# Kernel optimization log

Hardware: AMD Instinct MI355X
Metric: run time of the kernel (lower is better)

Reference implementation:

```python
import jax, jax.numpy as jnp
import numpy as np

DEPTH_BINS = 64
TEMPERATURE = 1.0


def _conv2d(x, w, b, pad):
    y = jax.lax.conv_general_dilated(x, w, (1, 1), [(pad, pad), (pad, pad)],
                                     dimension_numbers=('NCHW', 'OIHW', 'NCHW'))
    return y + b[None, :, None, None]


def _conv3d(x, w, b, pad):
    y = jax.lax.conv_general_dilated(x, w, (1, 1, 1), [(pad, pad)] * 3,
                                     dimension_numbers=('NCDHW', 'OIDHW', 'NCDHW'))
    return y + b[None, :, None, None, None]


def setup_inputs() -> dict:
    key = jax.random.key(0)
    ks = jax.random.split(key, 16)
    B, N, C, H, W = 2, 5, 256, 96, 96
    s = 0.05  # weight scale
    return {
        'focal_features': jax.random.normal(ks[0], (B, N, C, H, W), jnp.float32),
        'focus_distances': jax.random.uniform(ks[1], (B, N), jnp.float32, 0.5, 5.0),
        'camera_encoding': jax.random.normal(ks[2], (B, 16), jnp.float32),
        'W1': jax.random.normal(ks[3], (256, 512, 3, 3), jnp.float32) * s,
        'b1': jnp.zeros((256,), jnp.float32),
        'W2': jax.random.normal(ks[4], (128, 256, 3, 3), jnp.float32) * s,
        'b2': jnp.zeros((128,), jnp.float32),
        'W3': jax.random.normal(ks[5], (1, 128, 1, 1), jnp.float32) * s,
        'b3': jnp.zeros((1,), jnp.float32),
        'R1': jax.random.normal(ks[6], (32, 64, 3, 3, 3), jnp.float32) * s,
        'rb1': jnp.zeros((32,), jnp.float32),
        'R2': jax.random.normal(ks[7], (16, 32, 3, 3, 3), jnp.float32) * s,
        'rb2': jnp.zeros((16,), jnp.float32),
        'R3': jax.random.normal(ks[8], (64, 16, 1, 1, 1), jnp.float32) * s,
        'rb3': jnp.zeros((64,), jnp.float32),
    }


def reference(focal_features, focus_distances, camera_encoding,
              W1, b1, W2, b2, W3, b3, R1, rb1, R2, rb2, R3, rb3):
    B, N, C, H, W = focal_features.shape
    # _apply_blur is identity and depth only affects the (unused) blur sigma,
    # so the per-depth matching cost is identical across all depth bins.
    feat_ref = focal_features[:, 0]  # [B,C,H,W]
    pair = jnp.concatenate(
        [focal_features, jnp.broadcast_to(feat_ref[:, None], focal_features.shape)],
        axis=2)  # [B,N,2C,H,W]
    x = pair.reshape(B * N, 2 * C, H, W)
    x = jax.nn.relu(_conv2d(x, W1, b1, 1))
    x = jax.nn.relu(_conv2d(x, W2, b2, 1))
    cost = _conv2d(x, W3, b3, 0)  # [B*N,1,H,W]
    cost_agg = cost.reshape(B, N, H, W).mean(axis=1)  # [B,H,W]
    # identical for every depth bin -> broadcast
    cv = jnp.broadcast_to(cost_agg[:, None], (B, DEPTH_BINS, H, W))
    # refine_net: Conv3d over channels=depth_bins, spatial dims (H, W, 1)
    v = cv[..., None]  # [B, depth_bins, H, W, 1]
    v = jax.nn.relu(_conv3d(v, R1, rb1, 1))
    v = jax.nn.relu(_conv3d(v, R2, rb2, 1))
    v = _conv3d(v, R3, rb3, 0)  # [B, depth_bins, H, W, 1]
    cv_ref = v[..., 0]  # [B, depth_bins, H, W]
    depth_probs = jax.nn.softmax(-cv_ref / TEMPERATURE, axis=1)
    cost_volume = jnp.transpose(cv_ref, (0, 2, 3, 1))   # [B,H,W,depth_bins]
    depth_probs = jnp.transpose(depth_probs, (0, 2, 3, 1))
    return cost_volume, depth_probs
```

## Files before the change

### kernel.cpp

```cpp
#include <hip/hip_runtime.h>
#include <stdint.h>

typedef unsigned short u16;
typedef _Float16 f16;
typedef _Float16 f16x8 __attribute__((ext_vector_type(8)));
typedef float    f32x4 __attribute__((ext_vector_type(4)));

#define HW   96
#define NPIX (HW*HW)
#define BBATCH 2
#define NVIEW  5
#define NIMG 10

#define ASTR 80
#define LDS_B_OFF 7840
#define LDS_BYTES (7840 + 30720)

__device__ __forceinline__ u16 f16u(float f) {
    union { u16 u; f16 h; } v; v.h = (f16)f; return v.u;
}

__global__ __launch_bounds__(256)
void k_prep_w(const float* __restrict__ W1, const float* __restrict__ W2,
              const float* __restrict__ R1, const float* __restrict__ R2, const float* __restrict__ R3,
              u16* __restrict__ w1a, u16* __restrict__ w1b, u16* __restrict__ w2t,
              float* __restrict__ s1t, float* __restrict__ s2t, float* __restrict__ r3t)
{
    int id = blockIdx.x * 256 + threadIdx.x;
    if (id < 589824) {
        int t = id >> 16; int r = id & 65535; int o = r >> 8; int c = r & 255;
        int kh = t / 3, kw = t % 3;
        *(f16*)&w1a[id] = (f16)W1[((size_t)(o * 512 + c) * 3 + kh) * 3 + kw];
        *(f16*)&w1b[id] = (f16)W1[((size_t)(o * 512 + 256 + c) * 3 + kh) * 3 + kw];
        return;
    }
    id -= 589824;
    if (id < 294912) {
        int t = id >> 15; int r = id & 32767; int o = r >> 8; int c = r & 255;
        *(f16*)&w2t[id] = (f16)W2[((size_t)(o * 256 + c) * 3 + t / 3) * 3 + (t % 3)];
        return;
    }
    id -= 294912;
    if (id < 288) {
        int t = id >> 5; int o = id & 31;
        float s = 0.f;
        for (int i = 0; i < 64; ++i)
            s += R1[((size_t)((o * 64 + i) * 3 + t / 3) * 3 + t % 3) * 3 + 1];
        s1t[id] = s;
        return;
    }
    id -= 288;
    if (id < 4608) {
        int o = id & 15; int r = id >> 4; int i = r & 31; int t = r >> 5;
        s2t[id] = R2[((size_t)((o * 32 + i) * 3 + t / 3) * 3 + t % 3) * 3 + 1];
        return;
    }
    id -= 4608;
    if (id < 1024) {
        int o = id & 63; int i = id >> 6;
        r3t[id] = R3[(size_t)o * 16 + i];
    }
}

__global__ __launch_bounds__(256)
void k_tr(const float* __restrict__ src, u16* __restrict__ dst, int img0, int imgMul)
{
    const int cblk = blockIdx.x, row = blockIdx.y, z = blockIdx.z;
    const int gimg = img0 + z * imgMul;
    const int tid = threadIdx.x;
    __shared__ u16 tile[96 * 40];
    const int c = tid >> 3, j = tid & 7;
    const float* s = src + ((size_t)(gimg * 256 + cblk * 32 + c)) * NPIX + (size_t)row * HW + j * 12;
    #pragma unroll
    for (int k = 0; k < 3; ++k) {
        const float4 v = ((const float4*)s)[k];
        const int px = j * 12 + k * 4;
        tile[(px + 0) * 40 + c] = f16u(v.x);
        tile[(px + 1) * 40 + c] = f16u(v.y);
        tile[(px + 2) * 40 + c] = f16u(v.z);
        tile[(px + 3) * 40 + c] = f16u(v.w);
    }
    __syncthreads();
    if (tid < 192) {
        const int px = tid >> 1, part = tid & 1;
        const uint4 v0 = ((const uint4*)(tile + px * 40 + part * 16))[0];
        const uint4 v1 = ((const uint4*)(tile + px * 40 + part * 16))[1];
        uint4* d = (uint4*)(dst + ((((size_t)z * HW + row) * 8 + cblk) * HW + px) * 32 + part * 16);
        d[0] = v0; d[1] = v1;
    }
}

template<int MODE>
__global__ __launch_bounds__(256, 4)
void k_conv(const u16* __restrict__ in, const u16* __restrict__ wt,
            const u16* __restrict__ refp, const float* __restrict__ bias,
            const float* __restrict__ W3, void* __restrict__ outp, int ib)
{
    constexpr int Cout = (MODE == 2) ? 128 : 256;
    const int h  = blockIdx.x;
    const int y  = blockIdx.y;
    const int ob = blockIdx.z * 128;
    const int tid = threadIdx.x;
    const int wv = tid >> 6, l = tid & 63;
    const int wm = wv >> 1, wn = wv & 1;
    const int lane16 = l & 15, quad = l >> 4;

    __shared__ __align__(16) char lds[LDS_BYTES];

    f32x4 acc[3][4];
    #pragma unroll
    for (int mf = 0; mf < 3; ++mf)
        #pragma unroll
        for (int nf = 0; nf < 4; ++nf) acc[mf][nf] = (f32x4){0.f, 0.f, 0.f, 0.f};

    if (tid < 32) {
        const int base = (tid >> 4) ? 97 * ASTR : 0;
        ((unsigned int*)(lds + base))[tid & 15] = 0u;
    }

    for (int dh = -1; dh <= 1; ++dh) {
        const int hh = h + dh;
        if ((unsigned)hh >= (unsigned)HW) continue;
        for (int c0 = 0; c0 < 256; c0 += 32) {
            __syncthreads();
            if (tid < 192) {
                const int px = tid >> 1, half = tid & 1;
                const uint4* g = (const uint4*)(in +
                    ((((size_t)y * HW + hh) * 8 + (c0 >> 5)) * HW + px) * 32 + half * 16);
                const uint4 v0 = g[0], v1 = g[1];
                uint4* d = (uint4*)(lds + (px + 1) * ASTR + half * 32);
                d[0] = v0; d[1] = v1;
            }
            #pragma unroll
            for (int i = 0; i < 3; ++i) {
                const int idx = i * 256 + tid;
                const int dwt = idx >> 8, o = (idx >> 1) & 127, half = idx & 1;
                const int tap = (dh + 1) * 3 + dwt;
                const uint4* g = (const uint4*)(wt +
                    ((size_t)tap * Cout + ob + o) * 256 + c0 + half * 16);
                const uint4 v0 = g[0], v1 = g[1];
                uint4* d = (uint4*)(lds + LDS_B_OFF + (dwt * 128 + o) * ASTR + half * 32);
                d[0] = v0; d[1] = v1;
            }
            __syncthreads();
            #pragma unroll
            for (int dw = 0; dw < 3; ++dw) {
                f16x8 af[3];
                #pragma unroll
                for (int mf = 0; mf < 3; ++mf)
                    af[mf] = *(const f16x8*)(lds + (wm * 48 + mf * 16 + lane16 + dw) * ASTR + quad * 16);
                #pragma unroll
                for (int nf = 0; nf < 4; ++nf) {
                    const f16x8 bf = *(const f16x8*)(lds + LDS_B_OFF +
                        (dw * 128 + wn * 64 + nf * 16 + lane16) * ASTR + quad * 16);
                    #pragma unroll
                    for (int mf = 0; mf < 3; ++mf)
                        acc[mf][nf] = __builtin_amdgcn_mfma_f32_16x16x32_f16(af[mf], bf, acc[mf][nf], 0, 0, 0);
                }
            }
        }
    }

    if (MODE <= 1) {
        const int rimg = (MODE == 1) ? (ib + y) / NVIEW : 0;
        float bias4[4] = {0.f, 0.f, 0.f, 0.f};
        if (MODE == 1) {
            #pragma unroll
            for (int nf = 0; nf < 4; ++nf) bias4[nf] = bias[ob + wn * 64 + nf * 16 + lane16];
        }
        char* epi = lds + wv * 3072;
        u16* outg = (u16*)outp;
        #pragma unroll
        for (int p = 0; p < 2; ++p) {
            __syncthreads();
            #pragma unroll
            for (int nn = 0; nn < 2; ++nn) {
                const int nf = p * 2 + nn;
                #pragma unroll
                for (int mf = 0; mf < 3; ++mf)
                    #pragma unroll
                    for (int r = 0; r < 4; ++r) {
                        const int pxl = mf * 16 + quad * 4 + r;
                        *(u16*)(epi + pxl * 64 + (nn * 16 + lane16) * 2) =
                            f16u(acc[mf][nf][r] + bias4[nf]);
                    }
            }
            __syncthreads();
            const int cblk = (ob + wn * 64 + p * 32) >> 5;
            const size_t obase = (((size_t)y * HW + h) * 8 + cblk) * (size_t)(HW * 32);
            const size_t rbase = (((size_t)rimg * HW + h) * 8 + cblk) * (size_t)(HW * 32);
            #pragma unroll
            for (int i = 0; i < 3; ++i) {
                const int u = i * 64 + l;
                const int pxl = u >> 2, part = u & 3;
                f16x8 v = *(const f16x8*)(epi + pxl * 64 + part * 16);
                const int px = wm * 48 + pxl;
                if (MODE == 1) {
                    const f16x8 rv = *(const f16x8*)(refp + rbase + (size_t)px * 32 + part * 8);
                    #pragma unroll
                    for (int jj = 0; jj < 8; ++jj)
                        v[jj] = (f16)fmaxf((float)v[jj] + (float)rv[jj], 0.f);
                }
                *(f16x8*)(outg + obase + (size_t)px * 32 + part * 8) = v;
            }
        }
    } else {
        const int gimg = ib + y;
        float w3v[4], b2v[4];
        #pragma unroll
        for (int nf = 0; nf < 4; ++nf) {
            const int o = wn * 64 + nf * 16 + lane16;
            w3v[nf] = W3[o]; b2v[nf] = bias[o];
        }
        float s[3][4];
        #pragma unroll
        for (int mf = 0; mf < 3; ++mf)
            #pragma unroll
            for (int r = 0; r < 4; ++r) {
                float t = 0.f;
                #pragma unroll
                for (int nf = 0; nf < 4; ++nf)
                    t += w3v[nf] * fmaxf(acc[mf][nf][r] + b2v[nf], 0.f);
                s[mf][r] = t;
            }
        #pragma unroll
        for (int xb = 1; xb < 16; xb <<= 1)
            #pragma unroll
            for (int mf = 0; mf < 3; ++mf)
                #pragma unroll
                for (int r = 0; r < 4; ++r)
                    s[mf][r] += __shfl_xor(s[mf][r], xb);
        __syncthreads();
        float* cs = (float*)lds;
        if (wn == 0 && lane16 == 0) {
            #pragma unroll
            for (int mf = 0; mf < 3; ++mf)
                #pragma unroll
                for (int r = 0; r < 4; ++r)
                    cs[wm * 48 + mf * 16 + quad * 4 + r] = s[mf][r];
        }
        __syncthreads();
        if (wn == 1 && lane16 == 0) {
            float* pvp = (float*)outp + (size_t)gimg * NPIX + (size_t)h * HW;
            #pragma unroll
            for (int mf = 0; mf < 3; ++mf)
                #pragma unroll
                for (int r = 0; r < 4; ++r) {
                    const int px = wm * 48 + mf * 16 + quad * 4 + r;
                    pvp[px] = cs[px] + s[mf][r];
                }
        }
    }
}

__global__ __launch_bounds__(256)
void k_cost_sum(const float* __restrict__ pv, const float* __restrict__ b3, float* __restrict__ ca)
{
    const int id = blockIdx.x * 256 + threadIdx.x;
    if (id >= BBATCH * NPIX) return;
    const int b = id / NPIX, hw = id % NPIX;
    float s = 0.f;
    #pragma unroll
    for (int n = 0; n < NVIEW; ++n) s += pv[(size_t)(b * NVIEW + n) * NPIX + hw];
    ca[id] = b3[0] + 0.2f * s;
}

__global__ __launch_bounds__(256)
void k_d1(const float* __restrict__ cost_agg, const float* __restrict__ s1t,
          const float* __restrict__ rb1, float* __restrict__ t1)
{
    const int id = blockIdx.x * 256 + threadIdx.x;
    const int o = id & 31; const int r = id >> 5;
    const int hw = r % NPIX; const int bimg = r / NPIX;
    const int y = hw / HW, x = hw % HW;
    const float* ca = cost_agg + (size_t)bimg * NPIX;
    float s = rb1[o];
    #pragma unroll
    for (int t = 0; t < 9; ++t) {
        const int yy = y + t / 3 - 1, xx = x + t % 3 - 1;
        if ((unsigned)yy < HW && (unsigned)xx < HW)
            s += s1t[t * 32 + o] * ca[yy * HW + xx];
    }
    t1[id] = fmaxf(s, 0.f);
}

__global__ __launch_bounds__(256)
void k_d2(const float* __restrict__ t1, const float* __restrict__ s2t,
          const float* __restrict__ rb2, float* __restrict__ t2)
{
    const int id = blockIdx.x * 256 + threadIdx.x;
    const int o = id & 15; const int r = id >> 4;
    const int hw = r % NPIX; const int bimg = r / NPIX;
    const int y = hw / HW, x = hw % HW;
    float s = rb2[o];
    for (int t = 0; t < 9; ++t) {
        const int yy = y + t / 3 - 1, xx = x + t % 3 - 1;
        if ((unsigned)yy < HW && (unsigned)xx < HW) {
            const float* tp = t1 + ((size_t)bimg * NPIX + yy * HW + xx) * 32;
            #pragma unroll
            for (int i = 0; i < 32; ++i)
                s += s2t[(t * 32 + i) * 16 + o] * tp[i];
        }
    }
    t2[id] = fmaxf(s, 0.f);
}

__global__ __launch_bounds__(256)
void k_d3(const float* __restrict__ t2, const float* __restrict__ r3t,
          const float* __restrict__ rb3, float* __restrict__ out)
{
    const int wv = threadIdx.x >> 6, o = threadIdx.x & 63;
    const int pix = blockIdx.x * 4 + wv;
    const float* tp = t2 + (size_t)pix * 16;
    float cv = rb3[o];
    #pragma unroll
    for (int i = 0; i < 16; ++i) cv += r3t[i * 64 + o] * tp[i];
    const float z = -cv;
    float m = z;
    #pragma unroll
    for (int off = 32; off; off >>= 1) m = fmaxf(m, __shfl_xor(m, off));
    const float e = __expf(z - m);
    float s = e;
    #pragma unroll
    for (int off = 32; off; off >>= 1) s += __shfl_xor(s, off);
    const float p = e / s;
    const size_t idx = (size_t)pix * 64 + o;
    out[idx] = cv;
    out[idx + (size_t)BBATCH * NPIX * 64] = p;
}

extern "C" void kernel_launch(void* const* d_in, const int* in_sizes, int n_in,
                              void* d_out, int out_size, void* d_ws, size_t ws_size,
                              hipStream_t stream)
{
    (void)in_sizes; (void)n_in; (void)out_size;
    const float* focal = (const float*)d_in[0];
    const float* W1  = (const float*)d_in[3];
    const float* b1  = (const float*)d_in[4];
    const float* W2  = (const float*)d_in[5];
    const float* b2  = (const float*)d_in[6];
    const float* W3  = (const float*)d_in[7];
    const float* b3  = (const float*)d_in[8];
    const float* R1  = (const float*)d_in[9];
    const float* rb1 = (const float*)d_in[10];
    const float* R2  = (const float*)d_in[11];
    const float* rb2 = (const float*)d_in[12];
    const float* R3  = (const float*)d_in[13];
    const float* rb3 = (const float*)d_in[14];

    char* ws = (char*)d_ws;
    size_t off = 0;
    auto alloc = [&](size_t sz) { char* p = ws + off; off = (off + sz + 255) & ~(size_t)255; return p; };
    const size_t IMG = (size_t)HW * 8 * HW * 32 * 2;
    u16*   w1a  = (u16*)  alloc(1179648);
    u16*   w1b  = (u16*)  alloc(1179648);
    u16*   w2t  = (u16*)  alloc(589824);
    float* s1t  = (float*)alloc(1152);
    float* s2t  = (float*)alloc(18432);
    float* r3t  = (float*)alloc(4096);
    float* ca   = (float*)alloc(73728);
    float* t1   = (float*)alloc(2359296);
    float* t2   = (float*)alloc(1179648);
    float* pv   = (float*)alloc(NIMG * NPIX * 4);
    u16*   refp   = (u16*)alloc(BBATCH * IMG);
    u16*   feats2 = (u16*)alloc(BBATCH * IMG);
    const size_t base = off;
    int C = 1;
    if (base + 20 * IMG + 512 <= ws_size)      C = 10;
    else if (base + 10 * IMG + 512 <= ws_size) C = 5;
    else if (base + 4 * IMG + 512 <= ws_size)  C = 2;
    u16* feats = (u16*)alloc((size_t)C * IMG);
    u16* x1    = (u16*)alloc((size_t)C * IMG);

    k_prep_w<<<(890656 + 255) / 256, 256, 0, stream>>>(W1, W2, R1, R2, R3, w1a, w1b, w2t, s1t, s2t, r3t);

    k_tr<<<dim3(8, HW, BBATCH), 256, 0, stream>>>(focal, feats2, 0, NVIEW);
    k_conv<0><<<dim3(HW, BBATCH, 2), 256, 0, stream>>>(feats2, w1b, nullptr, nullptr, nullptr, refp, 0);

    for (int ib = 0; ib < NIMG; ib += C) {
        k_tr<<<dim3(8, HW, C), 256, 0, stream>>>(focal, feats, ib, 1);
        k_conv<1><<<dim3(HW, C, 2), 256, 0, stream>>>(feats, w1a, refp, b1, nullptr, x1, ib);
        k_conv<2><<<dim3(HW, C, 1), 256, 0, stream>>>(x1, w2t, nullptr, b2, W3, pv, ib);
    }

    k_cost_sum<<<(BBATCH * NPIX + 255) / 256, 256, 0, stream>>>(pv, b3, ca);
    k_d1<<<(BBATCH * NPIX * 32) / 256, 256, 0, stream>>>(ca, s1t, rb1, t1);
    k_d2<<<(BBATCH * NPIX * 16) / 256, 256, 0, stream>>>(t1, s2t, rb2, t2);
    k_d3<<<(BBATCH * NPIX) / 4, 256, 0, stream>>>(t2, r3t, rb3, (float*)d_out);
}
```

Measured before the change: 471.2 us.

## Double-buffer activation tiles and read conv weights directly from global memory

The implicit-GEMM conv mainloop now keeps two LDS activation buffers. The next channel chunk is prefetched into registers while the MFMAs run, which removes one barrier per iteration. Weight fragments are no longer staged through LDS; each wave loads them directly from global memory (relying on L1/L2 reuse), which shrinks LDS from about 38KB to about 15KB. The trade-off is more global load traffic and latency on the weight path in exchange for fewer syncs and more room for occupancy.

```diff
diff --git a/kernel.cpp b/kernel.cpp
--- a/kernel.cpp
+++ b/kernel.cpp
@@ -13,8 +13,8 @@
 #define NIMG 10
 
 #define ASTR 80
-#define LDS_B_OFF 7840
-#define LDS_BYTES (7840 + 30720)
+#define ABUF 7840
+#define LDS_BYTES (2*ABUF)
 
 __device__ __forceinline__ u16 f16u(float f) {
     union { u16 u; f16 h; } v; v.h = (f16)f; return v.u;
@@ -106,6 +106,8 @@
     const int lane16 = l & 15, quad = l >> 4;
 
     __shared__ __align__(16) char lds[LDS_BYTES];
+    char* const bufA = lds;
+    char* const bufB = lds + ABUF;
 
     f32x4 acc[3][4];
     #pragma unroll
@@ -113,52 +115,75 @@
         #pragma unroll
         for (int nf = 0; nf < 4; ++nf) acc[mf][nf] = (f32x4){0.f, 0.f, 0.f, 0.f};
 
-    if (tid < 32) {
-        const int base = (tid >> 4) ? 97 * ASTR : 0;
-        ((unsigned int*)(lds + base))[tid & 15] = 0u;
-    }
-
+    int hh0 = 0, hh1 = 0, hh2 = 0, tb0 = 0, tb1 = 0, tb2 = 0, nv = 0;
+    #pragma unroll
     for (int dh = -1; dh <= 1; ++dh) {
-        const int hh = h + dh;
-        if ((unsigned)hh >= (unsigned)HW) continue;
-        for (int c0 = 0; c0 < 256; c0 += 32) {
-            __syncthreads();
-            if (tid < 192) {
-                const int px = tid >> 1, half = tid & 1;
-                const uint4* g = (const uint4*)(in +
-                    ((((size_t)y * HW + hh) * 8 + (c0 >> 5)) * HW + px) * 32 + half * 16);
-                const uint4 v0 = g[0], v1 = g[1];
-                uint4* d = (uint4*)(lds + (px + 1) * ASTR + half * 32);
-                d[0] = v0; d[1] = v1;
+        const int q = h + dh;
+        if ((unsigned)q < (unsigned)HW) {
+            if (nv == 0)      { hh0 = q; tb0 = (dh + 1) * 3; }
+            else if (nv == 1) { hh1 = q; tb1 = (dh + 1) * 3; }
+            else              { hh2 = q; tb2 = (dh + 1) * 3; }
+            ++nv;
+        }
+    }
+    const int NIT = nv * 8;
+    auto hsel = [&](int k) { return k == 0 ? hh0 : (k == 1 ? hh1 : hh2); };
+    auto tsel = [&](int k) { return k == 0 ? tb0 : (k == 1 ? tb1 : tb2); };
+
+    const u16* const wq = wt + ((size_t)(ob + wn * 64 + lane16)) * 256 + quad * 8;
+
+    const int spx = tid >> 1, shalf = tid & 1;
+    uint4 sA, sB;
+
+    if (tid < 192) {
+        const uint4* g = (const uint4*)(in +
+            ((((size_t)y * HW + hsel(0)) * 8 + 0) * HW + spx) * 32 + shalf * 16);
+        sA = g[0]; sB = g[1];
+        uint4* d = (uint4*)(bufA + (spx + 1) * ASTR + shalf * 32);
+        d[0] = sA; d[1] = sB;
+    }
+    if (tid < 64) {
+        char* b = (tid & 32) ? bufB : bufA;
+        const int base = (tid & 16) ? 97 * ASTR : 0;
+        ((unsigned int*)(b + base))[tid & 15] = 0u;
+    }
+    __syncthreads();
+
+    auto body = [&](int i, char* buf, char* nbuf) {
+        const int kk = i >> 3, c0 = (i & 7) * 32;
+        const int tb = tsel(kk);
+        const bool pf = (i + 1 < NIT) && (tid < 192);
+        if (pf) {
+            const int k2 = (i + 1) >> 3, c2 = ((i + 1) & 7) * 32;
+            const uint4* g = (const uint4*)(in +
+                ((((size_t)y * HW + hsel(k2)) * 8 + (c2 >> 5)) * HW + spx) * 32 + shalf * 16);
+            sA = g[0]; sB = g[1];
+        }
+        #pragma unroll
+        for (int dw = 0; dw < 3; ++dw) {
+            f16x8 af[3];
+            #pragma unroll
+            for (int mf = 0; mf < 3; ++mf)
+                af[mf] = *(const f16x8*)(buf + (wm * 48 + mf * 16 + lane16 + dw) * ASTR + quad * 16);
+            const int wb = (tb + dw) * Cout * 256 + c0;
+            #pragma unroll
+            for (int nf = 0; nf < 4; ++nf) {
+                const f16x8 bf = *(const f16x8*)(wq + wb + nf * 16 * 256);
+                #pragma unroll
+                for (int mf = 0; mf < 3; ++mf)
+                    acc[mf][nf] = __builtin_amdgcn_mfma_f32_16x16x32_f16(af[mf], bf, acc[mf][nf], 0, 0, 0);
             }
-            #pragma unroll
-            for (int i = 0; i < 3; ++i) {
-                const int idx = i * 256 + tid;
-                const int dwt = idx >> 8, o = (idx >> 1) & 127, half = idx & 1;
-                const int tap = (dh + 1) * 3 + dwt;
-                const uint4* g = (const uint4*)(wt +
-                    ((size_t)tap * Cout + ob + o) * 256 + c0 + half * 16);
-                const uint4 v0 = g[0], v1 = g[1];
-                uint4* d = (uint4*)(lds + LDS_B_OFF + (dwt * 128 + o) * ASTR + half * 32);
-                d[0] = v0; d[1] = v1;
-            }
-            __syncthreads();
-            #pragma unroll
-            for (int dw = 0; dw < 3; ++dw) {
-                f16x8 af[3];
-                #pragma unroll
-                for (int mf = 0; mf < 3; ++mf)
-                    af[mf] = *(const f16x8*)(lds + (wm * 48 + mf * 16 + lane16 + dw) * ASTR + quad * 16);
-                #pragma unroll
-                for (int nf = 0; nf < 4; ++nf) {
-                    const f16x8 bf = *(const f16x8*)(lds + LDS_B_OFF +
-                        (dw * 128 + wn * 64 + nf * 16 + lane16) * ASTR + quad * 16);
-                    #pragma unroll
-                    for (int mf = 0; mf < 3; ++mf)
-                        acc[mf][nf] = __builtin_amdgcn_mfma_f32_16x16x32_f16(af[mf], bf, acc[mf][nf], 0, 0, 0);
-                }
-            }
-        }
+        }
+        if (pf) {
+            uint4* d = (uint4*)(nbuf + (spx + 1) * ASTR + shalf * 32);
+            d[0] = sA; d[1] = sB;
+        }
+        __syncthreads();
+    };
+
+    for (int i = 0; i < NIT; i += 2) {
+        body(i,     bufA, bufB);
+        body(i + 1, bufB, bufA);
     }
 
     if (MODE <= 1) {
```

After: 695.1 us. 1.48x slower.
